# Kernel tuning notes

Measured on AMD Instinct MI355X. Metric: run time of the kernel, lower is better.

## Reference

```python
import jax, jax.numpy as jnp
import numpy as np

D_MODEL = 2048
H_Q = 32
H_KV = 8
D_HEAD = D_MODEL // H_Q  # 64
Q_PER_KV = H_Q // H_KV   # 4
B, L = 2, 2048


def setup_inputs() -> dict:
    key = jax.random.key(0)
    kx, kq, kk, kv, ko = jax.random.split(key, 5)
    s = 0.02
    return {
        "x": jax.random.normal(kx, (B, L, D_MODEL), dtype=jnp.float32),
        "Wq": jax.random.normal(kq, (D_MODEL, D_MODEL), dtype=jnp.float32) * s,
        "Wk": jax.random.normal(kk, (D_MODEL, D_HEAD * H_KV), dtype=jnp.float32) * s,
        "Wv": jax.random.normal(kv, (D_MODEL, D_HEAD * H_KV), dtype=jnp.float32) * s,
        "Wo": jax.random.normal(ko, (D_MODEL, D_MODEL), dtype=jnp.float32) * s,
    }


def reference(x, Wq, Wk, Wv, Wo):
    Bb, Ll, _ = x.shape
    # Projections (nn.Linear with bias=False -> x @ W; weights stored as (in, out))
    Q = (x @ Wq).reshape(Bb, Ll, H_Q, D_HEAD)          # (B, L, Hq, d)
    K = (x @ Wk).reshape(Bb, Ll, H_KV, D_HEAD)         # (B, L, Hkv, d)
    V = (x @ Wv).reshape(Bb, Ll, H_KV, D_HEAD)
    # Group query heads: (B, Hkv, q_per_kv, L, d)
    Q = Q.transpose(0, 2, 1, 3).reshape(Bb, H_KV, Q_PER_KV, Ll, D_HEAD)
    K = K.transpose(0, 2, 1, 3)                        # (B, Hkv, L, d)
    V = V.transpose(0, 2, 1, 3)
    scale = 1.0 / jnp.sqrt(jnp.asarray(D_HEAD, dtype=x.dtype))
    # scores: (B, Hkv, q_per_kv, L, L)
    scores = jnp.einsum('bhgqd,bhkd->bhgqk', Q, K) * scale
    attn = jax.nn.softmax(scores, axis=-1)
    out = jnp.einsum('bhgqk,bhkd->bhgqd', attn, V)     # (B, Hkv, g, L, d)
    out = out.reshape(Bb, H_Q, Ll, D_HEAD).transpose(0, 2, 1, 3).reshape(Bb, Ll, D_MODEL)
    return out @ Wo
```

## Files before the change

### kernel.cpp

```cpp
#include <hip/hip_runtime.h>
#include <hip/hip_bf16.h>
#include <cstdint>

#define D_MODEL 2048
#define HQ 32
#define HKV 8
#define DH 64
#define NB 2
#define LSEQ 2048
#define MROWS (NB*LSEQ)
#define KVB 64

typedef __attribute__((ext_vector_type(8))) short short8;
typedef __attribute__((ext_vector_type(4))) short short4v;
typedef __attribute__((ext_vector_type(4))) float f32x4;
typedef __attribute__((ext_vector_type(4))) unsigned short ushort4v;
typedef __attribute__((ext_vector_type(4))) unsigned int uint4v;
typedef unsigned short ushort;

__device__ __forceinline__ ushort f2bf(float f) {
    unsigned u = __float_as_uint(f);
    u += 0x7fffu + ((u >> 16) & 1u);
    return (ushort)(u >> 16);
}

__device__ __forceinline__ float ex2(float x) {
    float r;
    asm volatile("v_exp_f32 %0, %1\n\ts_nop 0" : "=v"(r) : "v"(x));
    return r;
}

__device__ __forceinline__ unsigned cvtpk(float a, float b) {
    unsigned r;
    asm("v_cvt_pk_bf16_f32 %0, %1, %2" : "=v"(r) : "v"(a), "v"(b));
    return r;
}

__device__ __forceinline__ void gload_lds16(const ushort* gsrc, ushort* ldst) {
    __builtin_amdgcn_global_load_lds((const __attribute__((address_space(1))) void*)gsrc,
                                     (__attribute__((address_space(3))) void*)ldst, 16, 0, 0);
}

__global__ __launch_bounds__(256)
void cvt_bf16_k(const float* __restrict__ in, ushort* __restrict__ out, int n4) {
    int i = blockIdx.x * blockDim.x + threadIdx.x;
    if (i < n4) {
        float4 v = *(const float4*)(in + (size_t)i * 4);
        ushort4v o = {f2bf(v.x), f2bf(v.y), f2bf(v.z), f2bf(v.w)};
        *(ushort4v*)(out + (size_t)i * 4) = o;
    }
}

__global__ __launch_bounds__(256)
void transpose_cvt(const float* __restrict__ W, ushort* __restrict__ Wt, int Kd, int Nd) {
    __shared__ float t[32][33];
    const int tid = threadIdx.x;
    const int n0 = blockIdx.x * 32, k0 = blockIdx.y * 32;
    const int r = tid >> 3, c4 = (tid & 7) << 2;
    float4 v = *(const float4*)(W + (size_t)(k0 + r) * Nd + n0 + c4);
    t[r][c4 + 0] = v.x; t[r][c4 + 1] = v.y; t[r][c4 + 2] = v.z; t[r][c4 + 3] = v.w;
    __syncthreads();
    const int n = tid >> 3, kc = (tid & 7) << 2;
    ushort4v o = {f2bf(t[kc + 0][n]), f2bf(t[kc + 1][n]), f2bf(t[kc + 2][n]), f2bf(t[kc + 3][n])};
    *(ushort4v*)(Wt + (size_t)(n0 + n) * Kd + k0 + kc) = o;
}

template<int BM, int MODE>
__global__ __launch_bounds__(256, 2)
void gemm_bf16(const ushort* __restrict__ A, const ushort* __restrict__ Bt,
               void* __restrict__ Cv, int M, int N, int K, float scale)
{
    constexpr int BN = 128;
    constexpr int FM = BM / 32;
    constexpr int ISSA = BM / 64;
    __shared__ __align__(16) ushort smem[2 * (BM + BN) * 32];
    ushort* As = smem;
    ushort* Bs = smem + 2 * BM * 32;

    const int tid = threadIdx.x;
    const int w = tid >> 6;
    const int wr = w >> 1, wc = w & 1;
    const int g = (tid & 63) >> 4, r16 = tid & 15;
    const int bm = blockIdx.y * BM, bn = blockIdx.x * BN;
    const int srow = tid >> 2, sphys = tid & 3;

    f32x4 acc[FM][4];
#pragma unroll
    for (int i = 0; i < FM; ++i)
#pragma unroll
        for (int j = 0; j < 4; ++j) acc[i][j] = {0.f, 0.f, 0.f, 0.f};

    auto stage = [&](int buf, int k0) {
#pragma unroll
        for (int i = 0; i < ISSA; ++i) {
            int row = i * 64 + srow;
            int slog = sphys ^ ((row >> 1) & 3);
            gload_lds16(A + (size_t)(bm + row) * K + k0 + slog * 8,
                        As + buf * BM * 32 + (i * 64 + w * 16) * 32);
        }
#pragma unroll
        for (int i = 0; i < 2; ++i) {
            int row = i * 64 + srow;
            int slog = sphys ^ ((row >> 1) & 3);
            gload_lds16(Bt + (size_t)(bn + row) * K + k0 + slog * 8,
                        Bs + buf * 128 * 32 + (i * 64 + w * 16) * 32);
        }
    };

    const int NTk = K >> 5;
    stage(0, 0);
    __syncthreads();
    int buf = 0;
    for (int kt = 0; kt < NTk; ++kt) {
        if (kt + 1 < NTk) stage(buf ^ 1, (kt + 1) << 5);
        const ushort* Ab = As + buf * BM * 32;
        const ushort* Bb = Bs + buf * 128 * 32;
        short8 af[FM], bfv[4];
#pragma unroll
        for (int mi = 0; mi < FM; ++mi) {
            int row = wr * (BM / 2) + mi * 16 + r16;
            int p = g ^ ((row >> 1) & 3);
            af[mi] = *(const short8*)(Ab + row * 32 + p * 8);
        }
#pragma unroll
        for (int ni = 0; ni < 4; ++ni) {
            int row = wc * 64 + ni * 16 + r16;
            int p = g ^ ((row >> 1) & 3);
            bfv[ni] = *(const short8*)(Bb + row * 32 + p * 8);
        }
#pragma unroll
        for (int mi = 0; mi < FM; ++mi)
#pragma unroll
            for (int ni = 0; ni < 4; ++ni)
                acc[mi][ni] = __builtin_amdgcn_mfma_f32_16x16x32_bf16(af[mi], bfv[ni], acc[mi][ni], 0, 0, 0);
        __syncthreads();
        buf ^= 1;
    }

    float* C = (float*)Cv;
#pragma unroll
    for (int mi = 0; mi < FM; ++mi)
#pragma unroll
        for (int ni = 0; ni < 4; ++ni)
#pragma unroll
            for (int r = 0; r < 4; ++r) {
                int row = bm + wr * (BM / 2) + mi * 16 + g * 4 + r;
                int col = bn + wc * 64 + ni * 16 + r16;
                C[(size_t)row * N + col] = acc[mi][ni][r] * scale;
            }
}

__global__ __launch_bounds__(256, 2)
void gemm_qkv(const ushort* __restrict__ A, const ushort* __restrict__ Bt,
              ushort* __restrict__ Qd, ushort* __restrict__ Kd, ushort* __restrict__ Vd,
              float qscale)
{
    constexpr int K = 2048;
    __shared__ __align__(16) ushort smem[2 * 256 * 32];

    const int tid = threadIdx.x;
    const int l = tid & 63;
    const int w = tid >> 6;
    const int wr = w >> 1, wc = w & 1;
    const int g = l >> 4, r16 = l & 15;
    const int bm = blockIdx.y * 128, bn = blockIdx.x * 128;
    const int srow = tid >> 2, sphys = tid & 3;

    ushort* As = smem;
    ushort* Bs = smem + 2 * 128 * 32;

    f32x4 acc[4][4];
#pragma unroll
    for (int i = 0; i < 4; ++i)
#pragma unroll
        for (int j = 0; j < 4; ++j) acc[i][j] = {0.f, 0.f, 0.f, 0.f};

    auto stage = [&](int buf, int k0) {
#pragma unroll
        for (int i = 0; i < 2; ++i) {
            int row = i * 64 + srow;
            int slog = sphys ^ ((row >> 1) & 3);
            gload_lds16(A + (size_t)(bm + row) * K + k0 + slog * 8,
                        As + buf * 128 * 32 + (i * 64 + w * 16) * 32);
            gload_lds16(Bt + (size_t)(bn + row) * K + k0 + slog * 8,
                        Bs + buf * 128 * 32 + (i * 64 + w * 16) * 32);
        }
    };

    stage(0, 0);
    __syncthreads();
    int buf = 0;
    for (int kt = 0; kt < K / 32; ++kt) {
        if (kt + 1 < K / 32) stage(buf ^ 1, (kt + 1) << 5);
        const ushort* Ab = As + buf * 128 * 32;
        const ushort* Bb = Bs + buf * 128 * 32;
        short8 af[4], bfv[4];
#pragma unroll
        for (int mi = 0; mi < 4; ++mi) {
            int row = wr * 64 + mi * 16 + r16;
            int p = g ^ ((row >> 1) & 3);
            af[mi] = *(const short8*)(Ab + row * 32 + p * 8);
        }
#pragma unroll
        for (int ni = 0; ni < 4; ++ni) {
            int row = wc * 64 + ni * 16 + r16;
            int p = g ^ ((row >> 1) & 3);
            bfv[ni] = *(const short8*)(Bb + row * 32 + p * 8);
        }
#pragma unroll
        for (int mi = 0; mi < 4; ++mi)
#pragma unroll
            for (int ni = 0; ni < 4; ++ni)
                acc[mi][ni] = __builtin_amdgcn_mfma_f32_16x16x32_bf16(af[mi], bfv[ni], acc[mi][ni], 0, 0, 0);
        __syncthreads();
        buf ^= 1;
    }

    const int colbase = bn + wc * 64;
    const int rowbase = bm + wr * 64;
    const int b = rowbase >> 11;
    const int l0 = rowbase & (LSEQ - 1);
    ushort* Ls = smem + w * 64 * 64;
    __syncthreads();

    if (colbase < 2560) {
        const float sc = (colbase < 2048) ? qscale : 1.f;
#pragma unroll
        for (int mi = 0; mi < 4; ++mi)
#pragma unroll
            for (int ni = 0; ni < 4; ++ni)
#pragma unroll
                for (int r = 0; r < 4; ++r)
                    Ls[(mi * 16 + g * 4 + r) * 64 + ni * 16 + r16] = f2bf(acc[mi][ni][r] * sc);
        __syncthreads();
        ushort* dst;
        if (colbase < 2048)
            dst = Qd + (((size_t)(b * 32 + (colbase >> 6))) * LSEQ + l0) * 64;
        else
            dst = Kd + (((size_t)(b * 8 + ((colbase - 2048) >> 6))) * LSEQ + l0) * 64;
#pragma unroll
        for (int c = 0; c < 8; ++c) {
            int idx = c * 64 + l;
            *(short8*)(dst + idx * 8) = *(const short8*)(Ls + idx * 8);
        }
    } else {
#pragma unroll
        for (int mi = 0; mi < 4; ++mi)
#pragma unroll
            for (int ni = 0; ni < 4; ++ni)
#pragma unroll
                for (int r = 0; r < 4; ++r)
                    Ls[(ni * 16 + r16) * 64 + mi * 16 + g * 4 + r] = f2bf(acc[mi][ni][r]);
        __syncthreads();
        ushort* dst = Vd + (((size_t)(b * 8 + ((colbase - 2560) >> 6))) * 64 + l) * LSEQ + l0;
#pragma unroll
        for (int c = 0; c < 8; ++c)
            *(short8*)(dst + c * 8) = *(const short8*)(Ls + l * 64 + c * 8);
    }
}

__global__ __launch_bounds__(256, 2)
void attn_bf16(const ushort* __restrict__ Qb, const ushort* __restrict__ Kb,
               const ushort* __restrict__ Vtb, ushort* __restrict__ Ob)
{
    __shared__ __align__(16) ushort Ks[2][KVB * 64];
    __shared__ __align__(16) ushort Vs[2][64 * KVB];

    const int tid = threadIdx.x;
    const int l = tid & 63, w = tid >> 6;
    const int g = l >> 4, r16 = l & 15;
    const int bh = blockIdx.y, b = bh >> 5, hq = bh & 31, hk = hq >> 2;
    const int q0 = blockIdx.x * 128 + w * 32;

    const ushort* Qh = Qb + (size_t)bh * LSEQ * 64;
    const ushort* Kh = Kb + (size_t)(b * HKV + hk) * LSEQ * 64;
    const ushort* Vh = Vtb + (size_t)(b * HKV + hk) * 64 * LSEQ;

    short8 qf[2][2];
#pragma unroll
    for (int qb = 0; qb < 2; ++qb)
#pragma unroll
        for (int dh = 0; dh < 2; ++dh)
            qf[qb][dh] = *(const short8*)(Qh + (size_t)(q0 + qb * 16 + r16) * 64 + dh * 32 + g * 8);

    short8 ones;
#pragma unroll
    for (int j = 0; j < 8; ++j) ones[j] = (short)0x3F80;

    f32x4 acco[4][2];
#pragma unroll
    for (int i = 0; i < 4; ++i)
#pragma unroll
        for (int j = 0; j < 2; ++j) acco[i][j] = {0.f, 0.f, 0.f, 0.f};
    f32x4 accl[2] = {{0.f, 0.f, 0.f, 0.f}, {0.f, 0.f, 0.f, 0.f}};

    const int sr = tid >> 3, sp = tid & 7;

    auto stage = [&](ushort* kdst, ushort* vdst, int k0) {
        const int slog = sp ^ (sr & 7);
#pragma unroll
        for (int i = 0; i < 2; ++i)
            gload_lds16(Kh + (size_t)(k0 + i * 32 + sr) * 64 + slog * 8,
                        kdst + i * 2048 + w * 512);
#pragma unroll
        for (int i = 0; i < 2; ++i)
            gload_lds16(Vh + (size_t)(i * 32 + sr) * LSEQ + k0 + slog * 8,
                        vdst + i * 2048 + w * 512);
    };

    ushort* Kcur = Ks[0]; ushort* Knxt = Ks[1];
    ushort* Vcur = Vs[0]; ushort* Vnxt = Vs[1];
    stage(Kcur, Vcur, 0);
    __syncthreads();
    for (int kt = 0; kt < LSEQ / KVB; ++kt) {
        if (kt + 1 < LSEQ / KVB) stage(Knxt, Vnxt, (kt + 1) * KVB);

        f32x4 sacc[4][2];
#pragma unroll
        for (int kb = 0; kb < 4; ++kb) {
            const int row = kb * 16 + r16, c = r16 & 7;
            short8 kf0 = *(const short8*)(Kcur + row * 64 + ((g) ^ c) * 8);
            short8 kf1 = *(const short8*)(Kcur + row * 64 + ((4 + g) ^ c) * 8);
#pragma unroll
            for (int qb = 0; qb < 2; ++qb) {
                f32x4 z = {0.f, 0.f, 0.f, 0.f};
                z = __builtin_amdgcn_mfma_f32_16x16x32_bf16(kf0, qf[qb][0], z, 0, 0, 0);
                sacc[kb][qb] = __builtin_amdgcn_mfma_f32_16x16x32_bf16(kf1, qf[qb][1], z, 0, 0, 0);
            }
        }

        short8 vf[4][2];
#pragma unroll
        for (int db = 0; db < 4; ++db) {
            const int row = db * 16 + r16, c = r16 & 7;
#pragma unroll
            for (int s = 0; s < 2; ++s) {
                short4v lo = *(const short4v*)(Vcur + row * 64 + ((s * 4 + (g >> 1)) ^ c) * 8 + (g & 1) * 4);
                short4v hi = *(const short4v*)(Vcur + row * 64 + ((s * 4 + 2 + (g >> 1)) ^ c) * 8 + (g & 1) * 4);
                vf[db][s] = __builtin_shufflevector(lo, hi, 0, 1, 2, 3, 4, 5, 6, 7);
            }
        }

        short8 pf[2][2];
#pragma unroll
        for (int qb = 0; qb < 2; ++qb) {
            float p[16];
#pragma unroll
            for (int kb = 0; kb < 4; ++kb)
#pragma unroll
                for (int r = 0; r < 4; ++r)
                    p[kb * 4 + r] = ex2(sacc[kb][qb][r]);
#pragma unroll
            for (int s = 0; s < 2; ++s) {
                uint4v pu;
                pu[0] = cvtpk(p[s * 8 + 0], p[s * 8 + 1]);
                pu[1] = cvtpk(p[s * 8 + 2], p[s * 8 + 3]);
                pu[2] = cvtpk(p[s * 8 + 4], p[s * 8 + 5]);
                pu[3] = cvtpk(p[s * 8 + 6], p[s * 8 + 7]);
                pf[s][qb] = *(short8*)&pu;
            }
        }

#pragma unroll
        for (int db = 0; db < 4; ++db)
#pragma unroll
            for (int qb = 0; qb < 2; ++qb) {
                acco[db][qb] = __builtin_amdgcn_mfma_f32_16x16x32_bf16(vf[db][0], pf[0][qb], acco[db][qb], 0, 0, 0);
                acco[db][qb] = __builtin_amdgcn_mfma_f32_16x16x32_bf16(vf[db][1], pf[1][qb], acco[db][qb], 0, 0, 0);
            }
#pragma unroll
        for (int qb = 0; qb < 2; ++qb) {
            accl[qb] = __builtin_amdgcn_mfma_f32_16x16x32_bf16(ones, pf[0][qb], accl[qb], 0, 0, 0);
            accl[qb] = __builtin_amdgcn_mfma_f32_16x16x32_bf16(ones, pf[1][qb], accl[qb], 0, 0, 0);
        }

        __syncthreads();
        ushort* t;
        t = Kcur; Kcur = Knxt; Knxt = t;
        t = Vcur; Vcur = Vnxt; Vnxt = t;
    }

    float inv[2] = {1.f / accl[0][0], 1.f / accl[1][0]};
#pragma unroll
    for (int qb = 0; qb < 2; ++qb)
#pragma unroll
        for (int db = 0; db < 4; ++db) {
            int lseq = q0 + qb * 16 + r16;
            ushort4v o = {f2bf(acco[db][qb][0] * inv[qb]), f2bf(acco[db][qb][1] * inv[qb]),
                          f2bf(acco[db][qb][2] * inv[qb]), f2bf(acco[db][qb][3] * inv[qb])};
            *(ushort4v*)(Ob + ((size_t)b * LSEQ + lseq) * D_MODEL + hq * 64 + db * 16 + g * 4) = o;
        }
}

extern "C" void kernel_launch(void* const* d_in, const int* in_sizes, int n_in,
                              void* d_out, int out_size, void* d_ws, size_t ws_size,
                              hipStream_t stream)
{
    const float* x  = (const float*)d_in[0];
    const float* Wq = (const float*)d_in[1];
    const float* Wk = (const float*)d_in[2];
    const float* Wv = (const float*)d_in[3];
    const float* Wo = (const float*)d_in[4];

    ushort* xb  = (ushort*)d_ws;
    ushort* Ob  = xb;
    ushort* Wf  = xb  + (size_t)MROWS * D_MODEL;
    ushort* Wot = Wf  + (size_t)3072 * D_MODEL;
    ushort* Kbf = Wot + (size_t)D_MODEL * D_MODEL;
    ushort* Vtb = Kbf + (size_t)NB * HKV * LSEQ * DH;
    ushort* Qbf = (ushort*)d_out;

    dim3 blk(256);
    cvt_bf16_k<<<dim3((MROWS * D_MODEL / 4 + 255) / 256), blk, 0, stream>>>(x, xb, MROWS * D_MODEL / 4);
    transpose_cvt<<<dim3(D_MODEL / 32, D_MODEL / 32), blk, 0, stream>>>(Wq, Wf, D_MODEL, D_MODEL);
    transpose_cvt<<<dim3(512 / 32, D_MODEL / 32), blk, 0, stream>>>(Wk, Wf + (size_t)2048 * D_MODEL, D_MODEL, 512);
    transpose_cvt<<<dim3(512 / 32, D_MODEL / 32), blk, 0, stream>>>(Wv, Wf + (size_t)2560 * D_MODEL, D_MODEL, 512);
    transpose_cvt<<<dim3(D_MODEL / 32, D_MODEL / 32), blk, 0, stream>>>(Wo, Wot, D_MODEL, D_MODEL);

    gemm_qkv<<<dim3(3072 / 128, MROWS / 128), blk, 0, stream>>>(
        xb, Wf, Qbf, Kbf, Vtb, 0.125f * 1.44269504f);

    attn_bf16<<<dim3(LSEQ / 128, NB * HQ), blk, 0, stream>>>(Qbf, Kbf, Vtb, Ob);

    gemm_bf16<128, 0><<<dim3(D_MODEL / 128, MROWS / 128), blk, 0, stream>>>(
        Ob, Wot, d_out, MROWS, D_MODEL, D_MODEL, 1.f);
}
```

Before: 208.0 us.

## Store V in MFMA-fragment order, merge weight transposes, unroll attention double buffer

The QKV GEMM now writes V into a pre-swizzled, fragment-ordered layout. The attention kernel can then stage V with contiguous 16-byte global-to-LDS loads and read each V operand with a single 128-bit LDS load instead of two 64-bit loads and a shuffle. The four weight transpose launches are merged into one kernel that writes Wq/Wk/Wv/Wo into adjacent regions, which relies on Wot following Wf directly in the workspace. The attention KV loop is unrolled by two with fixed buffer pointers to drop the pointer swaps. Together these aim to cut LDS instruction count, launch overhead and strided V staging traffic.

```diff
diff --git a/kernel.cpp b/kernel.cpp
--- a/kernel.cpp
+++ b/kernel.cpp
@@ -12,7 +12,6 @@
 #define KVB 64
 
 typedef __attribute__((ext_vector_type(8))) short short8;
-typedef __attribute__((ext_vector_type(4))) short short4v;
 typedef __attribute__((ext_vector_type(4))) float f32x4;
 typedef __attribute__((ext_vector_type(4))) unsigned short ushort4v;
 typedef __attribute__((ext_vector_type(4))) unsigned int uint4v;
@@ -52,17 +51,24 @@
 }
 
 __global__ __launch_bounds__(256)
-void transpose_cvt(const float* __restrict__ W, ushort* __restrict__ Wt, int Kd, int Nd) {
+void transpose_all(const float* __restrict__ Wq, const float* __restrict__ Wk,
+                   const float* __restrict__ Wv, const float* __restrict__ Wo,
+                   ushort* __restrict__ dst) {
     __shared__ float t[32][33];
     const int tid = threadIdx.x;
     const int n0 = blockIdx.x * 32, k0 = blockIdx.y * 32;
+    const float* W; int Nd, nl;
+    if (n0 < 2048)      { W = Wq; Nd = 2048; nl = n0; }
+    else if (n0 < 2560) { W = Wk; Nd = 512;  nl = n0 - 2048; }
+    else if (n0 < 3072) { W = Wv; Nd = 512;  nl = n0 - 2560; }
+    else                { W = Wo; Nd = 2048; nl = n0 - 3072; }
     const int r = tid >> 3, c4 = (tid & 7) << 2;
-    float4 v = *(const float4*)(W + (size_t)(k0 + r) * Nd + n0 + c4);
+    float4 v = *(const float4*)(W + (size_t)(k0 + r) * Nd + nl + c4);
     t[r][c4 + 0] = v.x; t[r][c4 + 1] = v.y; t[r][c4 + 2] = v.z; t[r][c4 + 3] = v.w;
     __syncthreads();
     const int n = tid >> 3, kc = (tid & 7) << 2;
     ushort4v o = {f2bf(t[kc + 0][n]), f2bf(t[kc + 1][n]), f2bf(t[kc + 2][n]), f2bf(t[kc + 3][n])};
-    *(ushort4v*)(Wt + (size_t)(n0 + n) * Kd + k0 + kc) = o;
+    *(ushort4v*)(dst + (size_t)(n0 + n) * 2048 + k0 + kc) = o;
 }
 
 template<int BM, int MODE>
@@ -247,15 +253,19 @@
 #pragma unroll
         for (int mi = 0; mi < 4; ++mi)
 #pragma unroll
-            for (int ni = 0; ni < 4; ++ni)
-#pragma unroll
-                for (int r = 0; r < 4; ++r)
-                    Ls[(ni * 16 + r16) * 64 + mi * 16 + g * 4 + r] = f2bf(acc[mi][ni][r]);
+            for (int ni = 0; ni < 4; ++ni) {
+                ushort4v pk = {f2bf(acc[mi][ni][0]), f2bf(acc[mi][ni][1]),
+                               f2bf(acc[mi][ni][2]), f2bf(acc[mi][ni][3])};
+                *(ushort4v*)(&Ls[(((mi >> 1) * 64 + ni * 16 + r16) * 4 + g) * 8 + (mi & 1) * 4]) = pk;
+            }
         __syncthreads();
-        ushort* dst = Vd + (((size_t)(b * 8 + ((colbase - 2560) >> 6))) * 64 + l) * LSEQ + l0;
-#pragma unroll
-        for (int c = 0; c < 8; ++c)
-            *(short8*)(dst + c * 8) = *(const short8*)(Ls + l * 64 + c * 8);
+        const int h = (colbase - 2560) >> 6;
+        ushort* dst = Vd + (((size_t)(b * 8 + h)) * 64 + (l0 >> 5)) * 2048;
+#pragma unroll
+        for (int c = 0; c < 8; ++c) {
+            int idx = c * 64 + l;
+            *(short8*)(dst + (size_t)idx * 8) = *(const short8*)(Ls + idx * 8);
+        }
     }
 }
 
@@ -264,7 +274,7 @@
                const ushort* __restrict__ Vtb, ushort* __restrict__ Ob)
 {
     __shared__ __align__(16) ushort Ks[2][KVB * 64];
-    __shared__ __align__(16) ushort Vs[2][64 * KVB];
+    __shared__ __align__(16) ushort Vs[2][KVB * 64];
 
     const int tid = threadIdx.x;
     const int l = tid & 63, w = tid >> 6;
@@ -304,23 +314,19 @@
                         kdst + i * 2048 + w * 512);
 #pragma unroll
         for (int i = 0; i < 2; ++i)
-            gload_lds16(Vh + (size_t)(i * 32 + sr) * LSEQ + k0 + slog * 8,
+            gload_lds16(Vh + (size_t)k0 * 64 + i * 2048 + (size_t)tid * 8,
                         vdst + i * 2048 + w * 512);
     };
 
-    ushort* Kcur = Ks[0]; ushort* Knxt = Ks[1];
-    ushort* Vcur = Vs[0]; ushort* Vnxt = Vs[1];
-    stage(Kcur, Vcur, 0);
-    __syncthreads();
-    for (int kt = 0; kt < LSEQ / KVB; ++kt) {
-        if (kt + 1 < LSEQ / KVB) stage(Knxt, Vnxt, (kt + 1) * KVB);
+    auto body = [&](const ushort* Kc, const ushort* Vc, ushort* Kn, ushort* Vn, int t) {
+        if (t + 1 < LSEQ / KVB) stage(Kn, Vn, (t + 1) * KVB);
 
         f32x4 sacc[4][2];
 #pragma unroll
         for (int kb = 0; kb < 4; ++kb) {
             const int row = kb * 16 + r16, c = r16 & 7;
-            short8 kf0 = *(const short8*)(Kcur + row * 64 + ((g) ^ c) * 8);
-            short8 kf1 = *(const short8*)(Kcur + row * 64 + ((4 + g) ^ c) * 8);
+            short8 kf0 = *(const short8*)(Kc + row * 64 + ((g) ^ c) * 8);
+            short8 kf1 = *(const short8*)(Kc + row * 64 + ((4 + g) ^ c) * 8);
 #pragma unroll
             for (int qb = 0; qb < 2; ++qb) {
                 f32x4 z = {0.f, 0.f, 0.f, 0.f};
@@ -331,15 +337,10 @@
 
         short8 vf[4][2];
 #pragma unroll
-        for (int db = 0; db < 4; ++db) {
-            const int row = db * 16 + r16, c = r16 & 7;
-#pragma unroll
-            for (int s = 0; s < 2; ++s) {
-                short4v lo = *(const short4v*)(Vcur + row * 64 + ((s * 4 + (g >> 1)) ^ c) * 8 + (g & 1) * 4);
-                short4v hi = *(const short4v*)(Vcur + row * 64 + ((s * 4 + 2 + (g >> 1)) ^ c) * 8 + (g & 1) * 4);
-                vf[db][s] = __builtin_shufflevector(lo, hi, 0, 1, 2, 3, 4, 5, 6, 7);
-            }
-        }
+        for (int db = 0; db < 4; ++db)
+#pragma unroll
+            for (int s = 0; s < 2; ++s)
+                vf[db][s] = *(const short8*)(Vc + ((s * 64 + db * 16 + r16) * 4 + g) * 8);
 
         short8 pf[2][2];
 #pragma unroll
@@ -375,9 +376,13 @@
         }
 
         __syncthreads();
-        ushort* t;
-        t = Kcur; Kcur = Knxt; Knxt = t;
-        t = Vcur; Vcur = Vnxt; Vnxt = t;
+    };
+
+    stage(Ks[0], Vs[0], 0);
+    __syncthreads();
+    for (int kt = 0; kt < LSEQ / KVB; kt += 2) {
+        body(Ks[0], Vs[0], Ks[1], Vs[1], kt);
+        body(Ks[1], Vs[1], Ks[0], Vs[0], kt + 1);
     }
 
     float inv[2] = {1.f / accl[0][0], 1.f / accl[1][0]};
@@ -412,10 +417,7 @@
 
     dim3 blk(256);
     cvt_bf16_k<<<dim3((MROWS * D_MODEL / 4 + 255) / 256), blk, 0, stream>>>(x, xb, MROWS * D_MODEL / 4);
-    transpose_cvt<<<dim3(D_MODEL / 32, D_MODEL / 32), blk, 0, stream>>>(Wq, Wf, D_MODEL, D_MODEL);
-    transpose_cvt<<<dim3(512 / 32, D_MODEL / 32), blk, 0, stream>>>(Wk, Wf + (size_t)2048 * D_MODEL, D_MODEL, 512);
-    transpose_cvt<<<dim3(512 / 32, D_MODEL / 32), blk, 0, stream>>>(Wv, Wf + (size_t)2560 * D_MODEL, D_MODEL, 512);
-    transpose_cvt<<<dim3(D_MODEL / 32, D_MODEL / 32), blk, 0, stream>>>(Wo, Wot, D_MODEL, D_MODEL);
+    transpose_all<<<dim3(5120 / 32, D_MODEL / 32), blk, 0, stream>>>(Wq, Wk, Wv, Wo, Wf);
 
     gemm_qkv<<<dim3(3072 / 128, MROWS / 128), blk, 0, stream>>>(
         xb, Wf, Qbf, Kbf, Vtb, 0.125f * 1.44269504f);
```

Result: faster. 192.8 us (-7.3%).
